# Kernel tuning notes

Hardware: AMD Instinct MI355X
Metric: run time of the kernel (lower is better)

The kernel has to match this reference:

```python
import jax, jax.numpy as jnp
import numpy as np

N = 50000          # nodes
E = 800000         # random edges (self-loops added in reference, per PyG default)
B = 64             # graphs in batch
IN_DIM = 773
HID = 256
OUT = 128
H1, D1 = 4, 64     # heads, head_dim layer 1 (256 = 4*64)
H2, D2 = 4, 32     # heads, head_dim layer 2 (128 = 4*32)
NEG_SLOPE = 0.2


def setup_inputs() -> dict:
    key = jax.random.key(0)
    ks = jax.random.split(key, 20)
    s = 0.02
    x = jax.random.normal(ks[0], (N, IN_DIM), dtype=jnp.float32)
    edge_index = jax.random.randint(ks[1], (2, E), 0, N, dtype=jnp.int32)
    batch = jnp.sort(jax.random.randint(ks[2], (N,), 0, B, dtype=jnp.int32))
    return {
        "x": x,
        "edge_index": edge_index,
        "batch": batch,
        "W_in": jax.random.normal(ks[3], (IN_DIM, HID), jnp.float32) * s,
        "b_in": jnp.zeros((HID,), jnp.float32),
        "W1": jax.random.normal(ks[4], (HID, H1 * D1), jnp.float32) * s,
        "att_src1": jax.random.normal(ks[5], (H1, D1), jnp.float32) * s,
        "att_dst1": jax.random.normal(ks[6], (H1, D1), jnp.float32) * s,
        "b1": jnp.zeros((H1 * D1,), jnp.float32),
        "W2": jax.random.normal(ks[7], (HID, H2 * D2), jnp.float32) * s,
        "att_src2": jax.random.normal(ks[8], (H2, D2), jnp.float32) * s,
        "att_dst2": jax.random.normal(ks[9], (H2, D2), jnp.float32) * s,
        "b2": jnp.zeros((H2 * D2,), jnp.float32),
        "W_cls": jax.random.normal(ks[10], (OUT, 2), jnp.float32) * s,
        "b_cls": jnp.zeros((2,), jnp.float32),
        "W_conf": jax.random.normal(ks[11], (OUT, 1), jnp.float32) * s,
        "b_conf": jnp.zeros((1,), jnp.float32),
    }


def _gat_layer(h, src, dst, W, att_src, att_dst, bias, heads, dim):
    # h: (N, F_in). PyG GATConv, concat=True, eval mode (dropout off).
    hW = (h @ W).reshape(N, heads, dim)                    # (N, H, D)
    a_src = jnp.einsum("nhd,hd->nh", hW, att_src)          # (N, H)
    a_dst = jnp.einsum("nhd,hd->nh", hW, att_dst)
    e = a_src[src] + a_dst[dst]                            # (E', H)
    e = jax.nn.leaky_relu(e, NEG_SLOPE)
    # segment softmax over incoming edges of each dst node
    m = jax.ops.segment_max(e, dst, num_segments=N)        # (N, H)
    ex = jnp.exp(e - m[dst])
    z = jax.ops.segment_sum(ex, dst, num_segments=N)       # (N, H)
    alpha = ex / (z[dst] + 1e-16)                          # (E', H)
    msg = hW[src] * alpha[:, :, None]                      # (E', H, D)
    out = jax.ops.segment_sum(msg, dst, num_segments=N)    # (N, H, D)
    return out.reshape(N, heads * dim) + bias


def reference(x, edge_index, batch, W_in, b_in,
              W1, att_src1, att_dst1, b1,
              W2, att_src2, att_dst2, b2,
              W_cls, b_cls, W_conf, b_conf):
    loops = jnp.arange(N, dtype=edge_index.dtype)
    src = jnp.concatenate([edge_index[0], loops])
    dst = jnp.concatenate([edge_index[1], loops])

    h = jax.nn.relu(x @ W_in + b_in)                       # (N, 256)
    h = jax.nn.relu(_gat_layer(h, src, dst, W1, att_src1, att_dst1, b1, H1, D1))
    h = _gat_layer(h, src, dst, W2, att_src2, att_dst2, b2, H2, D2)
    h = jax.nn.relu(h)                                     # (N, 128)

    # global mean pool over graphs
    sums = jax.ops.segment_sum(h, batch, num_segments=B)   # (B, 128)
    cnts = jax.ops.segment_sum(jnp.ones((N,), h.dtype), batch, num_segments=B)
    graph_emb = sums / jnp.maximum(cnts, 1.0)[:, None]

    class_logits = graph_emb @ W_cls + b_cls               # (B, 2)
    confidence = jax.nn.sigmoid(graph_emb @ W_conf + b_conf)  # (B, 1)
    return class_logits, confidence
```

## Files before the change

kernel.cpp:

```cpp
#include <hip/hip_runtime.h>
#include <math.h>

#define NN 50000
#define NE 800000
#define NB 64
#define IND 773
#define MPAD 50048
#define SCAN_B 196

typedef __attribute__((ext_vector_type(8))) short short8_t;
typedef __attribute__((ext_vector_type(4))) float f32x4;

__device__ __forceinline__ float lrelu(float x) { return x > 0.f ? x : 0.2f * x; }
__device__ __forceinline__ short f2b(float f) {
    unsigned u = __float_as_uint(f);
    unsigned r = (u + 0x7fffu + ((u >> 16) & 1u)) >> 16;
    return (short)r;
}
__device__ __forceinline__ float b2f(short s) {
    return __uint_as_float(((unsigned)(unsigned short)s) << 16);
}

#define GLOAD16(g, l) __builtin_amdgcn_global_load_lds(                         \
    (const __attribute__((address_space(1))) void*)(g),                         \
    (__attribute__((address_space(3))) void*)(l), 16, 0, 0)

template<int RELU, int HASB>
__global__ __launch_bounds__(256) void gemm_lds(const short* __restrict__ A,
                                                const short* __restrict__ Bt,
                                                const float* __restrict__ bias,
                                                short* __restrict__ C,
                                                int M, int K, int N) {
    __shared__ short As[128 * 32];
    __shared__ short Bs[128 * 32];
    const int t = threadIdx.x;
    const int w = t >> 6, l = t & 63;
    const int l15 = l & 15, lh = l >> 4;
    const int bm = blockIdx.x * 128, bn = blockIdx.y * 128;
    const int wr = (w >> 1) * 64, wc = (w & 1) * 64;

    const short* aG = A + (size_t)(bm + w * 32 + (l >> 2)) * K + (l & 3) * 8;
    const short* bG = Bt + (size_t)(bn + w * 32 + (l >> 2)) * K + (l & 3) * 8;
    short* aL = As + (w * 32) * 32;
    short* bL = Bs + (w * 32) * 32;

    f32x4 acc[4][4];
#pragma unroll
    for (int i = 0; i < 4; ++i)
#pragma unroll
        for (int j = 0; j < 4; ++j) acc[i][j] = (f32x4){0.f, 0.f, 0.f, 0.f};

    for (int k0 = 0; k0 < K; k0 += 32) {
        __syncthreads();
        GLOAD16(aG + k0, aL);
        GLOAD16(aG + (size_t)16 * K + k0, aL + 16 * 32);
        GLOAD16(bG + k0, bL);
        GLOAD16(bG + (size_t)16 * K + k0, bL + 16 * 32);
        __syncthreads();
        short8_t af[4], bfr[4];
#pragma unroll
        for (int mi = 0; mi < 4; ++mi)
            af[mi] = *(const short8_t*)&As[(wr + mi * 16 + l15) * 32 + lh * 8];
#pragma unroll
        for (int ni = 0; ni < 4; ++ni)
            bfr[ni] = *(const short8_t*)&Bs[(wc + ni * 16 + l15) * 32 + lh * 8];
#pragma unroll
        for (int mi = 0; mi < 4; ++mi)
#pragma unroll
            for (int ni = 0; ni < 4; ++ni)
                acc[mi][ni] = __builtin_amdgcn_mfma_f32_16x16x32_bf16(af[mi], bfr[ni], acc[mi][ni], 0, 0, 0);
    }

#pragma unroll
    for (int mi = 0; mi < 4; ++mi) {
#pragma unroll
        for (int r = 0; r < 4; ++r) {
            int grow = bm + wr + mi * 16 + lh * 4 + r;
            if (grow >= M) continue;
#pragma unroll
            for (int ni = 0; ni < 4; ++ni) {
                int gcol = bn + wc + ni * 16 + l15;
                float v = acc[mi][ni][r];
                if (HASB) v += bias[gcol];
                if (RELU) v = fmaxf(v, 0.f);
                C[(size_t)grow * N + gcol] = f2b(v);
            }
        }
    }
}

__global__ __launch_bounds__(256) void k_cast_pad(const float* __restrict__ x,
                                                  short* __restrict__ xb) {
    int idx = blockIdx.x * 256 + threadIdx.x;
    if (idx >= NN * 50) return;
    int row = idx / 50;
    int c16 = idx - row * 50;
    int cb = c16 * 16;
    const float* xp = x + (size_t)row * IND + cb;
    short o[16];
    if (c16 < 48) {
        float v[16];
#pragma unroll
        for (int j = 0; j < 16; ++j) v[j] = xp[j];
#pragma unroll
        for (int j = 0; j < 16; ++j) o[j] = f2b(v[j]);
    } else if (c16 == 48) {
#pragma unroll
        for (int j = 0; j < 16; ++j) o[j] = (768 + j < IND) ? f2b(xp[j]) : (short)0;
    } else {
#pragma unroll
        for (int j = 0; j < 16; ++j) o[j] = 0;
    }
    short* dst = &xb[(size_t)row * 800 + cb];
    *(short8_t*)dst = *(short8_t*)&o[0];
    *(short8_t*)(dst + 8) = *(short8_t*)&o[8];
}

__global__ __launch_bounds__(256) void k_wt_t(const float* __restrict__ W,
                                              short* __restrict__ Wt,
                                              int K, int N, int Kp) {
    __shared__ short tile[32][33];
    int kb = blockIdx.x * 32, nb = blockIdx.y * 32;
    int tx = threadIdx.x & 31, ty = threadIdx.x >> 5;
#pragma unroll
    for (int r = 0; r < 32; r += 8) {
        int k = kb + ty + r;
        tile[ty + r][tx] = (k < K) ? f2b(W[(size_t)k * N + nb + tx]) : (short)0;
    }
    __syncthreads();
#pragma unroll
    for (int r = 0; r < 32; r += 8) {
        int n = nb + ty + r, k = kb + tx;
        Wt[(size_t)n * Kp + k] = tile[tx][ty + r];
    }
}

template<int HD>
__global__ __launch_bounds__(256) void att_dots(const short* __restrict__ hW,
                                                const float* __restrict__ att_s,
                                                const float* __restrict__ att_d,
                                                float* __restrict__ a_s,
                                                float* __restrict__ a_d) {
    const int CPL = HD / 64;
    int node = blockIdx.x * 4 + (threadIdx.x >> 6);
    int lane = threadIdx.x & 63;
    if (node >= NN) return;
    const short* row = hW + (size_t)node * HD + lane * CPL;
    float s = 0.f, d = 0.f;
#pragma unroll
    for (int j = 0; j < CPL; ++j) {
        float v = b2f(row[j]);
        s += v * att_s[lane * CPL + j];
        d += v * att_d[lane * CPL + j];
    }
#pragma unroll
    for (int off = 1; off < 16; off <<= 1) {
        s += __shfl_xor(s, off);
        d += __shfl_xor(d, off);
    }
    int h = lane >> 4;
    if ((lane & 15) == 0) {
        a_s[node * 4 + h] = s;
        a_d[node * 4 + h] = d;
    }
}

__global__ __launch_bounds__(256) void k_zero(int* __restrict__ p, int n) {
    int i = blockIdx.x * 256 + threadIdx.x;
    if (i < n) p[i] = 0;
}

__global__ void k_hist(const int* __restrict__ ei, int* __restrict__ deg) {
    int e = blockIdx.x * 256 + threadIdx.x;
    if (e >= NE) return;
    atomicAdd(&deg[ei[NE + e]], 1);
}

__global__ __launch_bounds__(256) void k_bsum(const int* __restrict__ deg,
                                              int* __restrict__ bsum) {
    int i = blockIdx.x * 256 + threadIdx.x;
    int v = (i < NN) ? deg[i] : 0;
#pragma unroll
    for (int off = 32; off; off >>= 1) v += __shfl_down(v, off);
    __shared__ int ws[4];
    if ((threadIdx.x & 63) == 0) ws[threadIdx.x >> 6] = v;
    __syncthreads();
    if (threadIdx.x == 0) bsum[blockIdx.x] = ws[0] + ws[1] + ws[2] + ws[3];
}

__global__ __launch_bounds__(256) void k_bscan(const int* __restrict__ bsum,
                                               int* __restrict__ boff) {
    int t = threadIdx.x;
    int orig = (t < SCAN_B) ? bsum[t] : 0;
    int v = orig;
    int lane = t & 63, wid = t >> 6;
#pragma unroll
    for (int off = 1; off < 64; off <<= 1) {
        int u = __shfl_up(v, off);
        if (lane >= off) v += u;
    }
    __shared__ int ws[4];
    if (lane == 63) ws[wid] = v;
    __syncthreads();
    int add = 0;
    for (int wq = 0; wq < wid; ++wq) add += ws[wq];
    if (t < SCAN_B) boff[t] = v + add - orig;
}

__global__ __launch_bounds__(256) void k_scan3(const int* __restrict__ deg,
                                               const int* __restrict__ boff,
                                               int* __restrict__ rowp,
                                               int* __restrict__ cursor) {
    int b = blockIdx.x;
    int i = b * 256 + threadIdx.x;
    int d = (i < NN) ? deg[i] : 0;
    int v = d;
    int lane = threadIdx.x & 63, wid = threadIdx.x >> 6;
#pragma unroll
    for (int off = 1; off < 64; off <<= 1) {
        int u = __shfl_up(v, off);
        if (lane >= off) v += u;
    }
    __shared__ int ws[4];
    if (lane == 63) ws[wid] = v;
    __syncthreads();
    int add = boff[b];
    for (int wq = 0; wq < wid; ++wq) add += ws[wq];
    int excl = add + v - d;
    if (i < NN) { rowp[i] = excl; cursor[i] = excl; }
    if (i == NN - 1) rowp[NN] = excl + d;
}

__global__ void k_scatter(const int* __restrict__ ei, int* __restrict__ cursor,
                          int* __restrict__ colidx) {
    int e = blockIdx.x * 256 + threadIdx.x;
    if (e >= NE) return;
    int s = ei[e], d = ei[NE + e];
    int pos = atomicAdd(&cursor[d], 1);
    colidx[pos] = s;
}

template<int HD>
__global__ __launch_bounds__(256) void gat_agg(const short* __restrict__ hW,
                                               const float* __restrict__ a_s,
                                               const float* __restrict__ a_d,
                                               const int* __restrict__ row_ptr,
                                               const int* __restrict__ colidx,
                                               const float* __restrict__ bias,
                                               short* __restrict__ outp) {
    const int CPL = HD / 64;
    int node = blockIdx.x * 4 + (threadIdx.x >> 6);
    int lane = threadIdx.x & 63;
    if (node >= NN) return;
    int h = lane >> 4;
    int start = row_ptr[node], end = row_ptr[node + 1];
    float adst = a_d[node * 4 + h];
    float eself = lrelu(a_s[node * 4 + h] + adst);

    float z = 1.f;
    float acc[CPL];
    {
        const short* row = hW + (size_t)node * HD + lane * CPL;
        if (CPL == 4) { short4 q = *(const short4*)row; acc[0]=b2f(q.x); acc[1]=b2f(q.y); acc[2]=b2f(q.z); acc[3]=b2f(q.w); }
        else          { short2 q = *(const short2*)row; acc[0]=b2f(q.x); acc[1]=b2f(q.y); }
    }
    for (int e = start; e < end; e += 8) {
        int sidx[8];
        float xs[8], ex[8];
#pragma unroll
        for (int q = 0; q < 8; ++q) {
            int ee = e + q;
            sidx[q] = colidx[ee < end ? ee : end - 1];
        }
#pragma unroll
        for (int q = 0; q < 8; ++q) xs[q] = a_s[sidx[q] * 4 + h];
        float v[8][CPL];
        if (CPL == 4) {
#pragma unroll
            for (int q = 0; q < 8; ++q) {
                short4 qq = *(const short4*)(hW + (size_t)sidx[q] * HD + lane * 4);
                v[q][0]=b2f(qq.x); v[q][1]=b2f(qq.y); v[q][2]=b2f(qq.z); v[q][3]=b2f(qq.w);
            }
        } else {
#pragma unroll
            for (int q = 0; q < 8; ++q) {
                short2 qq = *(const short2*)(hW + (size_t)sidx[q] * HD + lane * 2);
                v[q][0]=b2f(qq.x); v[q][1]=b2f(qq.y);
            }
        }
#pragma unroll
        for (int q = 0; q < 8; ++q) {
            float w = __expf(lrelu(xs[q] + adst) - eself);
            ex[q] = (e + q < end) ? w : 0.f;
        }
#pragma unroll
        for (int q = 0; q < 8; ++q) z += ex[q];
#pragma unroll
        for (int j = 0; j < CPL; ++j) {
            float a = 0.f;
#pragma unroll
            for (int q = 0; q < 8; ++q) a += ex[q] * v[q][j];
            acc[j] += a;
        }
    }
    float inv = 1.f / z;
    short* orow = outp + (size_t)node * HD + lane * CPL;
#pragma unroll
    for (int j = 0; j < CPL; ++j)
        orow[j] = f2b(fmaxf(acc[j] * inv + bias[lane * CPL + j], 0.f));
}

__global__ __launch_bounds__(512) void pool_head(const short* __restrict__ h2,
                                                 const int* __restrict__ batch,
                                                 const float* __restrict__ W_cls,
                                                 const float* __restrict__ b_cls,
                                                 const float* __restrict__ W_conf,
                                                 const float* __restrict__ b_conf,
                                                 float* __restrict__ out) {
    int b = blockIdx.x;
    int t = threadIdx.x & 127;
    int g = threadIdx.x >> 7;
    int lo = 0, hi = NN;
    while (lo < hi) { int mid = (lo + hi) >> 1; if (batch[mid] < b) lo = mid + 1; else hi = mid; }
    int start = lo;
    lo = 0; hi = NN;
    while (lo < hi) { int mid = (lo + hi) >> 1; if (batch[mid] < b + 1) lo = mid + 1; else hi = mid; }
    int end = lo;

    float acc = 0.f;
    for (int n = start + g; n < end; n += 4) acc += b2f(h2[(size_t)n * 128 + t]);
    __shared__ float se[4][128];
    se[g][t] = acc;
    __syncthreads();
    if (g == 0) {
        float emb = (se[0][t] + se[1][t] + se[2][t] + se[3][t]) /
                    fmaxf((float)(end - start), 1.f);
        se[0][t] = emb;
    }
    __syncthreads();
    if (threadIdx.x == 0) {
        float v = b_cls[0];
        for (int c = 0; c < 128; ++c) v += se[0][c] * W_cls[c * 2 + 0];
        out[b * 2 + 0] = v;
    } else if (threadIdx.x == 1) {
        float v = b_cls[1];
        for (int c = 0; c < 128; ++c) v += se[0][c] * W_cls[c * 2 + 1];
        out[b * 2 + 1] = v;
    } else if (threadIdx.x == 2) {
        float v = b_conf[0];
        for (int c = 0; c < 128; ++c) v += se[0][c] * W_conf[c];
        out[128 + b] = 1.f / (1.f + expf(-v));
    }
}

extern "C" void kernel_launch(void* const* d_in, const int* in_sizes, int n_in,
                              void* d_out, int out_size, void* d_ws, size_t ws_size,
                              hipStream_t stream) {
    const float* x        = (const float*)d_in[0];
    const int*   ei       = (const int*)d_in[1];
    const int*   batch    = (const int*)d_in[2];
    const float* W_in     = (const float*)d_in[3];
    const float* b_in     = (const float*)d_in[4];
    const float* W1       = (const float*)d_in[5];
    const float* att_src1 = (const float*)d_in[6];
    const float* att_dst1 = (const float*)d_in[7];
    const float* b1       = (const float*)d_in[8];
    const float* W2       = (const float*)d_in[9];
    const float* att_src2 = (const float*)d_in[10];
    const float* att_dst2 = (const float*)d_in[11];
    const float* b2       = (const float*)d_in[12];
    const float* W_cls    = (const float*)d_in[13];
    const float* b_cls    = (const float*)d_in[14];
    const float* W_conf   = (const float*)d_in[15];
    const float* b_conf   = (const float*)d_in[16];
    float* out = (float*)d_out;

    char* ws = (char*)d_ws;
    short* xb  = (short*)(ws + 0);
    short* hW1 = (short*)(ws + 0);
    short* h1  = (short*)(ws + 25624576);
    short* hW2 = (short*)(ws + 51249152);
    short* h2  = (short*)(ws + 64061440);
    short* h0  = (short*)(ws + 80076800);
    size_t base = 105701376;
    short* Wt_in = (short*)(ws + base);
    short* Wt1   = (short*)(ws + base + 409600);
    short* Wt2   = (short*)(ws + base + 540672);
    float* a_s1  = (float*)(ws + base + 606208);
    float* a_d1  = (float*)(ws + base + 1406208);
    int*   deg    = (int*)(ws + base + 2206208);
    int*   rowp   = (int*)(ws + base + 2406208);
    int*   cursor = (int*)(ws + base + 2606272);
    int*   colidx = (int*)(ws + base + 2806272);
    int*   bsum   = (int*)(ws + base + 6006272);
    int*   boff   = (int*)(ws + base + 6007296);

    k_wt_t<<<dim3(25, 8), 256, 0, stream>>>(W_in, Wt_in, IND, 256, 800);
    k_wt_t<<<dim3(8, 8), 256, 0, stream>>>(W1, Wt1, 256, 256, 256);
    k_wt_t<<<dim3(8, 4), 256, 0, stream>>>(W2, Wt2, 256, 128, 256);
    k_cast_pad<<<(NN * 50 + 255) / 256, 256, 0, stream>>>(x, xb);

    k_zero<<<SCAN_B, 256, 0, stream>>>(deg, NN);
    k_hist<<<NE / 256, 256, 0, stream>>>(ei, deg);
    k_bsum<<<SCAN_B, 256, 0, stream>>>(deg, bsum);
    k_bscan<<<1, 256, 0, stream>>>(bsum, boff);
    k_scan3<<<SCAN_B, 256, 0, stream>>>(deg, boff, rowp, cursor);
    k_scatter<<<NE / 256, 256, 0, stream>>>(ei, cursor, colidx);

    gemm_lds<1, 1><<<dim3(391, 2), 256, 0, stream>>>(xb, Wt_in, b_in, h0, NN, 800, 256);
    gemm_lds<0, 0><<<dim3(391, 2), 256, 0, stream>>>(h0, Wt1, nullptr, hW1, NN, 256, 256);
    att_dots<256><<<12500, 256, 0, stream>>>(hW1, att_src1, att_dst1, a_s1, a_d1);
    gat_agg<256><<<12500, 256, 0, stream>>>(hW1, a_s1, a_d1, rowp, colidx, b1, h1);
    gemm_lds<0, 0><<<dim3(391, 1), 256, 0, stream>>>(h1, Wt2, nullptr, hW2, NN, 256, 128);
    att_dots<128><<<12500, 256, 0, stream>>>(hW2, att_src2, att_dst2, a_s1, a_d1);
    gat_agg<128><<<12500, 256, 0, stream>>>(hW2, a_s1, a_d1, rowp, colidx, b2, h2);
    pool_head<<<NB, 512, 0, stream>>>(h2, batch, W_cls, b_cls, W_conf, b_conf, out);
}
```

Baseline: 425.7 us.

## Fuse input cast into first GEMM and attention dots into GAT GEMM epilogues

Removes the separate fp32-to-bf16 cast/pad kernel by having the first GEMM read fp32 x directly and convert while staging into LDS. It also computes the per-head attention dot products in the epilogues of the layer-1 and layer-2 GEMMs, dropping both att_dots kernels. The first two GEMMs now use full-N 256-wide tiles with 512 threads, so each A tile is loaded once. The costs are fewer blocks (391) per launch and unvectorized, strided fp32 loads of x in the first GEMM that are no longer asynchronous LDS copies.

```diff
diff --git a/kernel.cpp b/kernel.cpp
--- a/kernel.cpp
+++ b/kernel.cpp
@@ -25,22 +25,172 @@
     (const __attribute__((address_space(1))) void*)(g),                         \
     (__attribute__((address_space(3))) void*)(l), 16, 0, 0)
 
-template<int RELU, int HASB>
-__global__ __launch_bounds__(256) void gemm_lds(const short* __restrict__ A,
-                                                const short* __restrict__ Bt,
-                                                const float* __restrict__ bias,
-                                                short* __restrict__ C,
-                                                int M, int K, int N) {
+__global__ __launch_bounds__(512) void gemm_a(const float* __restrict__ X,
+                                              const short* __restrict__ Bt,
+                                              const float* __restrict__ bias,
+                                              short* __restrict__ C) {
+    const int K = 800, N = 256;
+    __shared__ short As[128 * 32];
+    __shared__ short Bs[256 * 32];
+    const int t = threadIdx.x;
+    const int w = t >> 6, l = t & 63;
+    const int l15 = l & 15, lh = l >> 4;
+    const int bm = blockIdx.x * 128;
+    const int wr = (w >> 2) * 64, wc = (w & 3) * 64;
+
+    const short* bG = Bt + (size_t)(t >> 2) * K + (t & 3) * 8;
+    short* bLu = Bs + w * 512;
+
+    f32x4 acc[4][4];
+#pragma unroll
+    for (int i = 0; i < 4; ++i)
+#pragma unroll
+        for (int j = 0; j < 4; ++j) acc[i][j] = (f32x4){0.f, 0.f, 0.f, 0.f};
+
+    for (int k0 = 0; k0 < K; k0 += 32) {
+        __syncthreads();
+        GLOAD16(bG + k0, bLu);
+        GLOAD16(bG + (size_t)128 * K + k0, bLu + 128 * 32);
+#pragma unroll
+        for (int i = 0; i < 4; ++i) {
+            int fid = i * 512 + t;
+            int row = fid >> 4;
+            int cp = fid & 15;
+            int gm = bm + row;
+            int gk = k0 + cp * 2;
+            const float* xp = X + (size_t)gm * IND + gk;
+            bool rowok = (gm < NN);
+            float v0 = (rowok && gk < IND) ? xp[0] : 0.f;
+            float v1 = (rowok && gk + 1 < IND) ? xp[1] : 0.f;
+            unsigned pk = ((unsigned)(unsigned short)f2b(v0)) |
+                          (((unsigned)(unsigned short)f2b(v1)) << 16);
+            *(unsigned*)&As[row * 32 + cp * 2] = pk;
+        }
+        __syncthreads();
+        short8_t af[4], bfr[4];
+#pragma unroll
+        for (int mi = 0; mi < 4; ++mi)
+            af[mi] = *(const short8_t*)&As[(wr + mi * 16 + l15) * 32 + lh * 8];
+#pragma unroll
+        for (int ni = 0; ni < 4; ++ni)
+            bfr[ni] = *(const short8_t*)&Bs[(wc + ni * 16 + l15) * 32 + lh * 8];
+#pragma unroll
+        for (int mi = 0; mi < 4; ++mi)
+#pragma unroll
+            for (int ni = 0; ni < 4; ++ni)
+                acc[mi][ni] = __builtin_amdgcn_mfma_f32_16x16x32_bf16(af[mi], bfr[ni], acc[mi][ni], 0, 0, 0);
+    }
+#pragma unroll
+    for (int mi = 0; mi < 4; ++mi) {
+#pragma unroll
+        for (int r = 0; r < 4; ++r) {
+            int grow = bm + wr + mi * 16 + lh * 4 + r;
+            if (grow >= NN) continue;
+#pragma unroll
+            for (int ni = 0; ni < 4; ++ni) {
+                int gcol = wc + ni * 16 + l15;
+                float v = fmaxf(acc[mi][ni][r] + bias[gcol], 0.f);
+                C[(size_t)grow * N + gcol] = f2b(v);
+            }
+        }
+    }
+}
+
+__global__ __launch_bounds__(512) void gemm_b(const short* __restrict__ A,
+                                              const short* __restrict__ Bt,
+                                              const float* __restrict__ att_s,
+                                              const float* __restrict__ att_d,
+                                              short* __restrict__ C,
+                                              float* __restrict__ a_s,
+                                              float* __restrict__ a_d) {
+    const int K = 256, N = 256;
+    __shared__ short As[128 * 32];
+    __shared__ short Bs[256 * 32];
+    const int t = threadIdx.x;
+    const int w = t >> 6, l = t & 63;
+    const int l15 = l & 15, lh = l >> 4;
+    const int bm = blockIdx.x * 128;
+    const int wr = (w >> 2) * 64, wc = (w & 3) * 64;
+
+    const short* aG = A + (size_t)(bm + (t >> 2)) * K + (t & 3) * 8;
+    const short* bG = Bt + (size_t)(t >> 2) * K + (t & 3) * 8;
+    short* aLu = As + w * 512;
+    short* bLu = Bs + w * 512;
+
+    f32x4 acc[4][4];
+#pragma unroll
+    for (int i = 0; i < 4; ++i)
+#pragma unroll
+        for (int j = 0; j < 4; ++j) acc[i][j] = (f32x4){0.f, 0.f, 0.f, 0.f};
+
+    for (int k0 = 0; k0 < K; k0 += 32) {
+        __syncthreads();
+        GLOAD16(aG + k0, aLu);
+        GLOAD16(bG + k0, bLu);
+        GLOAD16(bG + (size_t)128 * K + k0, bLu + 128 * 32);
+        __syncthreads();
+        short8_t af[4], bfr[4];
+#pragma unroll
+        for (int mi = 0; mi < 4; ++mi)
+            af[mi] = *(const short8_t*)&As[(wr + mi * 16 + l15) * 32 + lh * 8];
+#pragma unroll
+        for (int ni = 0; ni < 4; ++ni)
+            bfr[ni] = *(const short8_t*)&Bs[(wc + ni * 16 + l15) * 32 + lh * 8];
+#pragma unroll
+        for (int mi = 0; mi < 4; ++mi)
+#pragma unroll
+            for (int ni = 0; ni < 4; ++ni)
+                acc[mi][ni] = __builtin_amdgcn_mfma_f32_16x16x32_bf16(af[mi], bfr[ni], acc[mi][ni], 0, 0, 0);
+    }
+    const int head = wc >> 6;
+    float sa[4], sd[4];
+#pragma unroll
+    for (int ni = 0; ni < 4; ++ni) {
+        sa[ni] = att_s[head * 64 + ni * 16 + l15];
+        sd[ni] = att_d[head * 64 + ni * 16 + l15];
+    }
+#pragma unroll
+    for (int mi = 0; mi < 4; ++mi) {
+#pragma unroll
+        for (int r = 0; r < 4; ++r) {
+            int grow = bm + wr + mi * 16 + lh * 4 + r;
+            float s = acc[mi][0][r] * sa[0] + acc[mi][1][r] * sa[1] +
+                      acc[mi][2][r] * sa[2] + acc[mi][3][r] * sa[3];
+            float d = acc[mi][0][r] * sd[0] + acc[mi][1][r] * sd[1] +
+                      acc[mi][2][r] * sd[2] + acc[mi][3][r] * sd[3];
+#pragma unroll
+            for (int off = 1; off < 16; off <<= 1) {
+                s += __shfl_xor(s, off);
+                d += __shfl_xor(d, off);
+            }
+            if (grow < NN) {
+                if (l15 == 0) { a_s[grow * 4 + head] = s; a_d[grow * 4 + head] = d; }
+#pragma unroll
+                for (int ni = 0; ni < 4; ++ni)
+                    C[(size_t)grow * N + wc + ni * 16 + l15] = f2b(acc[mi][ni][r]);
+            }
+        }
+    }
+}
+
+__global__ __launch_bounds__(256) void gemm_c(const short* __restrict__ A,
+                                              const short* __restrict__ Bt,
+                                              const float* __restrict__ att_s,
+                                              const float* __restrict__ att_d,
+                                              short* __restrict__ C,
+                                              float* __restrict__ a_s,
+                                              float* __restrict__ a_d) {
+    const int K = 256, N = 128;
     __shared__ short As[128 * 32];
     __shared__ short Bs[128 * 32];
     const int t = threadIdx.x;
     const int w = t >> 6, l = t & 63;
     const int l15 = l & 15, lh = l >> 4;
-    const int bm = blockIdx.x * 128, bn = blockIdx.y * 128;
+    const int bm = blockIdx.x * 128;
     const int wr = (w >> 1) * 64, wc = (w & 1) * 64;
 
     const short* aG = A + (size_t)(bm + w * 32 + (l >> 2)) * K + (l & 3) * 8;
-    const short* bG = Bt + (size_t)(bn + w * 32 + (l >> 2)) * K + (l & 3) * 8;
+    const short* bG = Bt + (size_t)(w * 32 + (l >> 2)) * K + (l & 3) * 8;
     short* aL = As + (w * 32) * 32;
     short* bL = Bs + (w * 32) * 32;
 
@@ -70,50 +220,39 @@
             for (int ni = 0; ni < 4; ++ni)
                 acc[mi][ni] = __builtin_amdgcn_mfma_f32_16x16x32_bf16(af[mi], bfr[ni], acc[mi][ni], 0, 0, 0);
     }
-
+    const int h0 = wc >> 5;
+    float sa[4], sd[4];
+#pragma unroll
+    for (int ni = 0; ni < 4; ++ni) {
+        int idx = (h0 + (ni >> 1)) * 32 + (ni & 1) * 16 + l15;
+        sa[ni] = att_s[idx];
+        sd[ni] = att_d[idx];
+    }
 #pragma unroll
     for (int mi = 0; mi < 4; ++mi) {
 #pragma unroll
         for (int r = 0; r < 4; ++r) {
             int grow = bm + wr + mi * 16 + lh * 4 + r;
-            if (grow >= M) continue;
-#pragma unroll
-            for (int ni = 0; ni < 4; ++ni) {
-                int gcol = bn + wc + ni * 16 + l15;
-                float v = acc[mi][ni][r];
-                if (HASB) v += bias[gcol];
-                if (RELU) v = fmaxf(v, 0.f);
-                C[(size_t)grow * N + gcol] = f2b(v);
-            }
-        }
-    }
-}
-
-__global__ __launch_bounds__(256) void k_cast_pad(const float* __restrict__ x,
-                                                  short* __restrict__ xb) {
-    int idx = blockIdx.x * 256 + threadIdx.x;
-    if (idx >= NN * 50) return;
-    int row = idx / 50;
-    int c16 = idx - row * 50;
-    int cb = c16 * 16;
-    const float* xp = x + (size_t)row * IND + cb;
-    short o[16];
-    if (c16 < 48) {
-        float v[16];
-#pragma unroll
-        for (int j = 0; j < 16; ++j) v[j] = xp[j];
-#pragma unroll
-        for (int j = 0; j < 16; ++j) o[j] = f2b(v[j]);
-    } else if (c16 == 48) {
-#pragma unroll
-        for (int j = 0; j < 16; ++j) o[j] = (768 + j < IND) ? f2b(xp[j]) : (short)0;
-    } else {
-#pragma unroll
-        for (int j = 0; j < 16; ++j) o[j] = 0;
-    }
-    short* dst = &xb[(size_t)row * 800 + cb];
-    *(short8_t*)dst = *(short8_t*)&o[0];
-    *(short8_t*)(dst + 8) = *(short8_t*)&o[8];
+            float s0 = acc[mi][0][r] * sa[0] + acc[mi][1][r] * sa[1];
+            float s1 = acc[mi][2][r] * sa[2] + acc[mi][3][r] * sa[3];
+            float d0 = acc[mi][0][r] * sd[0] + acc[mi][1][r] * sd[1];
+            float d1 = acc[mi][2][r] * sd[2] + acc[mi][3][r] * sd[3];
+#pragma unroll
+            for (int off = 1; off < 16; off <<= 1) {
+                s0 += __shfl_xor(s0, off); s1 += __shfl_xor(s1, off);
+                d0 += __shfl_xor(d0, off); d1 += __shfl_xor(d1, off);
+            }
+            if (grow < NN) {
+                if (l15 == 0) {
+                    a_s[grow * 4 + h0] = s0; a_s[grow * 4 + h0 + 1] = s1;
+                    a_d[grow * 4 + h0] = d0; a_d[grow * 4 + h0 + 1] = d1;
+                }
+#pragma unroll
+                for (int ni = 0; ni < 4; ++ni)
+                    C[(size_t)grow * N + wc + ni * 16 + l15] = f2b(acc[mi][ni][r]);
+            }
+        }
+    }
 }
 
 __global__ __launch_bounds__(256) void k_wt_t(const float* __restrict__ W,
@@ -132,36 +271,6 @@
     for (int r = 0; r < 32; r += 8) {
         int n = nb + ty + r, k = kb + tx;
         Wt[(size_t)n * Kp + k] = tile[tx][ty + r];
-    }
-}
-
-template<int HD>
-__global__ __launch_bounds__(256) void att_dots(const short* __restrict__ hW,
-                                                const float* __restrict__ att_s,
-                                                const float* __restrict__ att_d,
-                                                float* __restrict__ a_s,
-                                                float* __restrict__ a_d) {
-    const int CPL = HD / 64;
-    int node = blockIdx.x * 4 + (threadIdx.x >> 6);
-    int lane = threadIdx.x & 63;
-    if (node >= NN) return;
-    const short* row = hW + (size_t)node * HD + lane * CPL;
-    float s = 0.f, d = 0.f;
-#pragma unroll
-    for (int j = 0; j < CPL; ++j) {
-        float v = b2f(row[j]);
-        s += v * att_s[lane * CPL + j];
-        d += v * att_d[lane * CPL + j];
-    }
-#pragma unroll
-    for (int off = 1; off < 16; off <<= 1) {
-        s += __shfl_xor(s, off);
-        d += __shfl_xor(d, off);
-    }
-    int h = lane >> 4;
-    if ((lane & 15) == 0) {
-        a_s[node * 4 + h] = s;
-        a_d[node * 4 + h] = d;
     }
 }
 
@@ -376,13 +485,12 @@
     float* out = (float*)d_out;
 
     char* ws = (char*)d_ws;
-    short* xb  = (short*)(ws + 0);
-    short* hW1 = (short*)(ws + 0);
-    short* h1  = (short*)(ws + 25624576);
-    short* hW2 = (short*)(ws + 51249152);
-    short* h2  = (short*)(ws + 64061440);
-    short* h0  = (short*)(ws + 80076800);
-    size_t base = 105701376;
+    short* h0  = (short*)(ws + 0);
+    short* hW1 = (short*)(ws + 25624576);
+    short* h1  = (short*)(ws + 51249152);
+    short* hW2 = (short*)(ws + 76873728);
+    short* h2  = (short*)(ws + 89686016);
+    size_t base = 102498304;
     short* Wt_in = (short*)(ws + base);
     short* Wt1   = (short*)(ws + base + 409600);
     short* Wt2   = (short*)(ws + base + 540672);
@@ -398,7 +506,6 @@
     k_wt_t<<<dim3(25, 8), 256, 0, stream>>>(W_in, Wt_in, IND, 256, 800);
     k_wt_t<<<dim3(8, 8), 256, 0, stream>>>(W1, Wt1, 256, 256, 256);
     k_wt_t<<<dim3(8, 4), 256, 0, stream>>>(W2, Wt2, 256, 128, 256);
-    k_cast_pad<<<(NN * 50 + 255) / 256, 256, 0, stream>>>(x, xb);
 
     k_zero<<<SCAN_B, 256, 0, stream>>>(deg, NN);
     k_hist<<<NE / 256, 256, 0, stream>>>(ei, deg);
@@ -407,12 +514,10 @@
     k_scan3<<<SCAN_B, 256, 0, stream>>>(deg, boff, rowp, cursor);
     k_scatter<<<NE / 256, 256, 0, stream>>>(ei, cursor, colidx);
 
-    gemm_lds<1, 1><<<dim3(391, 2), 256, 0, stream>>>(xb, Wt_in, b_in, h0, NN, 800, 256);
-    gemm_lds<0, 0><<<dim3(391, 2), 256, 0, stream>>>(h0, Wt1, nullptr, hW1, NN, 256, 256);
-    att_dots<256><<<12500, 256, 0, stream>>>(hW1, att_src1, att_dst1, a_s1, a_d1);
+    gemm_a<<<391, 512, 0, stream>>>(x, Wt_in, b_in, h0);
+    gemm_b<<<391, 512, 0, stream>>>(h0, Wt1, att_src1, att_dst1, hW1, a_s1, a_d1);
     gat_agg<256><<<12500, 256, 0, stream>>>(hW1, a_s1, a_d1, rowp, colidx, b1, h1);
-    gemm_lds<0, 0><<<dim3(391, 1), 256, 0, stream>>>(h1, Wt2, nullptr, hW2, NN, 256, 128);
-    att_dots<128><<<12500, 256, 0, stream>>>(hW2, att_src2, att_dst2, a_s1, a_d1);
+    gemm_c<<<391, 256, 0, stream>>>(h1, Wt2, att_src2, att_dst2, hW2, a_s1, a_d1);
     gat_agg<128><<<12500, 256, 0, stream>>>(hW2, a_s1, a_d1, rowp, colidx, b2, h2);
     pool_head<<<NB, 512, 0, stream>>>(h2, batch, W_cls, b_cls, W_conf, b_conf, out);
 }
```

Result: faster. 409.3 us (-3.8%).
